# Performance work log

Hardware: AMD Instinct MI355X
Metric: run time of the kernel (lower is better)

The kernel has to match this reference:

```python
import jax, jax.numpy as jnp
import numpy as np

NUM_USER = 262144
NUM_ITEM = 262144
DIM = 64
NNZ = 1_250_000
N_LAYERS = 3


def setup_inputs() -> dict:
    key = jax.random.key(0)
    ku, ki, kr, kc, kv = jax.random.split(key, 5)
    n = NUM_USER + NUM_ITEM
    # xavier_uniform bound for (rows, cols) weight
    a = float(np.sqrt(6.0 / (NUM_USER + DIM)))
    user_emb = jax.random.uniform(ku, (NUM_USER, DIM), minval=-a, maxval=a, dtype=jnp.float32)
    b = float(np.sqrt(6.0 / (NUM_ITEM + DIM)))
    item_emb = jax.random.uniform(ki, (NUM_ITEM, DIM), minval=-b, maxval=b, dtype=jnp.float32)
    adj_rows = jax.random.randint(kr, (NNZ,), 0, n, dtype=jnp.int32)
    adj_cols = jax.random.randint(kc, (NNZ,), 0, n, dtype=jnp.int32)
    # normalized adjacency values are small positive floats
    adj_vals = jax.random.uniform(kv, (NNZ,), minval=0.0, maxval=0.1, dtype=jnp.float32)
    return {"user_emb": user_emb, "item_emb": item_emb,
            "adj_rows": adj_rows, "adj_cols": adj_cols, "adj_vals": adj_vals}


def reference(user_emb, item_emb, adj_rows, adj_cols, adj_vals):
    num_user = user_emb.shape[0]
    ego = jnp.concatenate([user_emb, item_emb], axis=0)  # [N, D]
    n = ego.shape[0]

    def spmm(x):
        # sparse.mm(adj, x): gather source rows, scale, scatter-add to dest rows
        msgs = adj_vals[:, None] * x[adj_cols]            # [NNZ, D]
        return jax.ops.segment_sum(msgs, adj_rows, num_segments=n)

    # running sum instead of stack+mean (same math: mean over L+1 layer outputs)
    acc = ego
    cur = ego
    for _ in range(N_LAYERS):
        cur = spmm(cur)
        acc = acc + cur
    mean_emb = acc / jnp.asarray(N_LAYERS + 1, dtype=ego.dtype)
    return mean_emb[:num_user], mean_emb[num_user:]
```

## Files before the change

### kernel.cpp

```cpp
#include <hip/hip_runtime.h>


constexpr int NUM_USER = 262144;
constexpr int NUM_ITEM = 262144;
constexpr int DIM      = 64;
constexpr int N_NODES  = NUM_USER + NUM_ITEM;
constexpr int NNZ      = 1250000;

constexpr int NBUCK = 256;
constexpr int ROWS_PER_BUCK = N_NODES / NBUCK;
constexpr int PB_BLOCKS = 512;
constexpr int CHUNK = 2444;
constexpr int BCAP = 6144;

typedef float  __f4 __attribute__((ext_vector_type(4)));

__device__ __forceinline__ unsigned bfpack2(float a, float b) {
    unsigned ua = __float_as_uint(a); ua += 0x7fffu + ((ua >> 16) & 1u);
    unsigned ub = __float_as_uint(b); ub += 0x7fffu + ((ub >> 16) & 1u);
    return (ua >> 16) | (ub & 0xffff0000u);
}
__device__ __forceinline__ uint4 bfpack8(float4 a, float4 b) {
    return make_uint4(bfpack2(a.x, a.y), bfpack2(a.z, a.w),
                      bfpack2(b.x, b.y), bfpack2(b.z, b.w));
}
__device__ __forceinline__ void bfunpack8(uint4 u, float4& l, float4& h) {
    l.x = __uint_as_float(u.x << 16);
    l.y = __uint_as_float(u.x & 0xffff0000u);
    l.z = __uint_as_float(u.y << 16);
    l.w = __uint_as_float(u.y & 0xffff0000u);
    h.x = __uint_as_float(u.z << 16);
    h.y = __uint_as_float(u.z & 0xffff0000u);
    h.z = __uint_as_float(u.w << 16);
    h.w = __uint_as_float(u.w & 0xffff0000u);
}
__device__ __forceinline__ void fma4(float4& s, float v, const float4 x) {
    s.x = fmaf(v, x.x, s.x);
    s.y = fmaf(v, x.y, s.y);
    s.z = fmaf(v, x.z, s.z);
    s.w = fmaf(v, x.w, s.w);
}
__device__ __forceinline__ float4 add4(float4 a, float4 b) {
    return make_float4(a.x + b.x, a.y + b.y, a.z + b.z, a.w + b.w);
}

__global__ void bucket_count(const int* __restrict__ rows, int* __restrict__ bcnt) {
    __shared__ int lcnt[NBUCK];
    const int t = threadIdx.x;
    lcnt[t] = 0;
    __syncthreads();
    const int beg = blockIdx.x * CHUNK;
    const int end = min(beg + CHUNK, NNZ);
    const int n    = max(end - beg, 0);
    const int nvec = n >> 2;
    const int4* rows4 = (const int4*)(rows + beg);
    for (int i = t; i < nvec; i += 256) {
        const int4 r = rows4[i];
        atomicAdd(&lcnt[r.x >> 11], 1);
        atomicAdd(&lcnt[r.y >> 11], 1);
        atomicAdd(&lcnt[r.z >> 11], 1);
        atomicAdd(&lcnt[r.w >> 11], 1);
    }
    if (t < (n & 3)) atomicAdd(&lcnt[rows[beg + (nvec << 2) + t] >> 11], 1);
    __syncthreads();
    bcnt[t * PB_BLOCKS + blockIdx.x] = lcnt[t];
}

__global__ void scan_bcnt(int* __restrict__ bcnt, int* __restrict__ tot) {
    __shared__ int tmp[256];
    const int b = blockIdx.x, t = threadIdx.x;
    const int a0 = bcnt[b * PB_BLOCKS + 2 * t];
    const int a1 = bcnt[b * PB_BLOCKS + 2 * t + 1];
    const int run = a0 + a1;
    tmp[t] = run;
    __syncthreads();
    for (int off = 1; off < 256; off <<= 1) {
        int x = (t >= off) ? tmp[t - off] : 0;
        __syncthreads();
        tmp[t] += x;
        __syncthreads();
    }
    const int excl = tmp[t] - run;
    bcnt[b * PB_BLOCKS + 2 * t]     = excl;
    bcnt[b * PB_BLOCKS + 2 * t + 1] = excl + a0;
    if (t == 255) tot[b] = tmp[255];
}

__global__ void scan_btot(const int* __restrict__ tot, int* __restrict__ bbase) {
    __shared__ int tmp[256];
    const int t = threadIdx.x;
    const int v = tot[t];
    tmp[t] = v;
    __syncthreads();
    for (int off = 1; off < 256; off <<= 1) {
        int x = (t >= off) ? tmp[t - off] : 0;
        __syncthreads();
        tmp[t] += x;
        __syncthreads();
    }
    bbase[t] = tmp[t] - v;
    if (t == 0) bbase[NBUCK] = NNZ;
}

__global__ void bucket_scatter(const int* __restrict__ rows, const int* __restrict__ cols,
                               const float* __restrict__ vals,
                               const int* __restrict__ bcnt, const int* __restrict__ bbase,
                               int2* __restrict__ eb, unsigned short* __restrict__ ebrow) {
    __shared__ int lbase[NBUCK];
    __shared__ int lofs[NBUCK];
    const int t = threadIdx.x;
    lbase[t] = bbase[t] + bcnt[t * PB_BLOCKS + blockIdx.x];
    lofs[t] = 0;
    __syncthreads();
    const int beg = blockIdx.x * CHUNK;
    const int end = min(beg + CHUNK, NNZ);
    const int n    = max(end - beg, 0);
    const int nvec = n >> 2;
    const int4*   rows4 = (const int4*)(rows + beg);
    const int4*   cols4 = (const int4*)(cols + beg);
    const float4* vals4 = (const float4*)(vals + beg);
    for (int i = t; i < nvec; i += 256) {
        const int4   r = rows4[i];
        const int4   c = cols4[i];
        const float4 v = vals4[i];
        int b, p;
        b = r.x >> 11; p = lbase[b] + atomicAdd(&lofs[b], 1);
        eb[p] = make_int2(c.x, __float_as_int(v.x));
        ebrow[p] = (unsigned short)(r.x & (ROWS_PER_BUCK - 1));
        b = r.y >> 11; p = lbase[b] + atomicAdd(&lofs[b], 1);
        eb[p] = make_int2(c.y, __float_as_int(v.y));
        ebrow[p] = (unsigned short)(r.y & (ROWS_PER_BUCK - 1));
        b = r.z >> 11; p = lbase[b] + atomicAdd(&lofs[b], 1);
        eb[p] = make_int2(c.z, __float_as_int(v.z));
        ebrow[p] = (unsigned short)(r.z & (ROWS_PER_BUCK - 1));
        b = r.w >> 11; p = lbase[b] + atomicAdd(&lofs[b], 1);
        eb[p] = make_int2(c.w, __float_as_int(v.w));
        ebrow[p] = (unsigned short)(r.w & (ROWS_PER_BUCK - 1));
    }
    if (t < (n & 3)) {
        const int i = beg + (nvec << 2) + t;
        const int r = rows[i];
        const int b = r >> 11;
        const int p = lbase[b] + atomicAdd(&lofs[b], 1);
        eb[p] = make_int2(cols[i], __float_as_int(vals[i]));
        ebrow[p] = (unsigned short)(r & (ROWS_PER_BUCK - 1));
    }
}

__global__ void bucket_finalize(const int* __restrict__ bbase,
                                const int2* __restrict__ eb,
                                const unsigned short* __restrict__ ebrow,
                                int* __restrict__ row_ptr, int2* __restrict__ sc) {
    __shared__ int  lcnt[ROWS_PER_BUCK];
    __shared__ int  tmp[256];
    __shared__ int2 lout[BCAP];
    const int b    = blockIdx.x;
    const int t    = threadIdx.x;
    const int base = bbase[b];
    const int cnt  = bbase[b + 1] - base;
    for (int r = t; r < ROWS_PER_BUCK; r += 256) lcnt[r] = 0;
    __syncthreads();
    for (int i = t; i < cnt; i += 256)
        atomicAdd(&lcnt[ebrow[base + i]], 1);
    __syncthreads();
    int loc[8];
    int run = 0;
    #pragma unroll
    for (int k = 0; k < 8; ++k) { const int v = lcnt[t * 8 + k]; loc[k] = run; run += v; }
    tmp[t] = run;
    __syncthreads();
    for (int off = 1; off < 256; off <<= 1) {
        int x = (t >= off) ? tmp[t - off] : 0;
        __syncthreads();
        tmp[t] += x;
        __syncthreads();
    }
    const int excl = tmp[t] - run;
    #pragma unroll
    for (int k = 0; k < 8; ++k) lcnt[t * 8 + k] = loc[k] + excl;
    __syncthreads();
    for (int r = t; r < ROWS_PER_BUCK; r += 256)
        row_ptr[b * ROWS_PER_BUCK + r] = base + lcnt[r];
    if (b == NBUCK - 1 && t == 0) row_ptr[N_NODES] = NNZ;
    __syncthreads();
    if (cnt <= BCAP) {
        for (int i = t; i < cnt; i += 256) {
            const int p = atomicAdd(&lcnt[ebrow[base + i]], 1);
            lout[p] = eb[base + i];
        }
        __syncthreads();
        for (int i = t; i < cnt; i += 256)
            sc[base + i] = lout[i];
    } else {
        for (int i = t; i < cnt; i += 256) {
            const int p = atomicAdd(&lcnt[ebrow[base + i]], 1);
            sc[base + p] = eb[base + i];
        }
    }
}

__global__ void spmm_first(const int* __restrict__ ptr, const int2* __restrict__ sc,
                           const float4* __restrict__ ue4, const float4* __restrict__ ie4,
                           uint4* __restrict__ e1b) {
    const int row = blockIdx.x * 32 + (threadIdx.x >> 3);
    const int d8  = threadIdx.x & 7;
    const int beg = ptr[row];
    const int end = ptr[row + 1];
    float4 a0 = {0.f,0.f,0.f,0.f}, b0 = {0.f,0.f,0.f,0.f};
    float4 a1 = {0.f,0.f,0.f,0.f}, b1 = {0.f,0.f,0.f,0.f};
    int e = beg;
    for (; e + 2 <= end; e += 2) {
        const int2 A = sc[e];
        const int2 B = sc[e + 1];
        const float4* pa = (A.x < NUM_USER) ? ue4 + (size_t)A.x * 16
                                            : ie4 + (size_t)(A.x - NUM_USER) * 16;
        const float4* pb = (B.x < NUM_USER) ? ue4 + (size_t)B.x * 16
                                            : ie4 + (size_t)(B.x - NUM_USER) * 16;
        const float4 al = pa[2 * d8], ah = pa[2 * d8 + 1];
        const float4 bl = pb[2 * d8], bh = pb[2 * d8 + 1];
        const float va = __int_as_float(A.y);
        const float vb = __int_as_float(B.y);
        fma4(a0, va, al); fma4(b0, va, ah);
        fma4(a1, vb, bl); fma4(b1, vb, bh);
    }
    if (e < end) {
        const int2 A = sc[e];
        const float4* pa = (A.x < NUM_USER) ? ue4 + (size_t)A.x * 16
                                            : ie4 + (size_t)(A.x - NUM_USER) * 16;
        const float va = __int_as_float(A.y);
        fma4(a0, va, pa[2 * d8]); fma4(b0, va, pa[2 * d8 + 1]);
    }
    e1b[row * 8 + d8] = bfpack8(add4(a0, a1), add4(b0, b1));
}

__global__ void spmm_b2b(const int* __restrict__ ptr, const int2* __restrict__ sc,
                         const uint4* __restrict__ xb, uint4* __restrict__ yb) {
    const int row = blockIdx.x * 32 + (threadIdx.x >> 3);
    const int d8  = threadIdx.x & 7;
    const int beg = ptr[row];
    const int end = ptr[row + 1];
    float4 a0 = {0.f,0.f,0.f,0.f}, b0 = {0.f,0.f,0.f,0.f};
    float4 a1 = {0.f,0.f,0.f,0.f}, b1 = {0.f,0.f,0.f,0.f};
    int e = beg;
    for (; e + 2 <= end; e += 2) {
        const int2 A = sc[e];
        const int2 B = sc[e + 1];
        const uint4 xa = xb[A.x * 8 + d8];
        const uint4 xc = xb[B.x * 8 + d8];
        float4 l, h;
        bfunpack8(xa, l, h);
        fma4(a0, __int_as_float(A.y), l); fma4(b0, __int_as_float(A.y), h);
        bfunpack8(xc, l, h);
        fma4(a1, __int_as_float(B.y), l); fma4(b1, __int_as_float(B.y), h);
    }
    if (e < end) {
        const int2 A = sc[e];
        float4 l, h;
        bfunpack8(xb[A.x * 8 + d8], l, h);
        fma4(a0, __int_as_float(A.y), l); fma4(b0, __int_as_float(A.y), h);
    }
    yb[row * 8 + d8] = bfpack8(add4(a0, a1), add4(b0, b1));
}

__global__ void spmm_last(const int* __restrict__ ptr, const int2* __restrict__ sc,
                          const float4* __restrict__ ue4, const float4* __restrict__ ie4,
                          const uint4* __restrict__ e1b, const uint4* __restrict__ e2b,
                          float4* __restrict__ out4) {
    const int row = blockIdx.x * 32 + (threadIdx.x >> 3);
    const int d8  = threadIdx.x & 7;
    const int beg = ptr[row];
    const int end = ptr[row + 1];
    const int o8 = row * 8 + d8;
    const float4* pg = (row < NUM_USER) ? ue4 + (size_t)row * 16
                                        : ie4 + (size_t)(row - NUM_USER) * 16;
    const float4 gl = pg[2 * d8];
    const float4 gh = pg[2 * d8 + 1];
    const uint4 u1 = e1b[o8];
    const uint4 u2 = e2b[o8];
    float4 a0 = {0.f,0.f,0.f,0.f}, b0 = {0.f,0.f,0.f,0.f};
    float4 a1 = {0.f,0.f,0.f,0.f}, b1 = {0.f,0.f,0.f,0.f};
    int e = beg;
    for (; e + 2 <= end; e += 2) {
        const int2 A = sc[e];
        const int2 B = sc[e + 1];
        const uint4 xa = e2b[A.x * 8 + d8];
        const uint4 xc = e2b[B.x * 8 + d8];
        float4 l, h;
        bfunpack8(xa, l, h);
        fma4(a0, __int_as_float(A.y), l); fma4(b0, __int_as_float(A.y), h);
        bfunpack8(xc, l, h);
        fma4(a1, __int_as_float(B.y), l); fma4(b1, __int_as_float(B.y), h);
    }
    if (e < end) {
        const int2 A = sc[e];
        float4 l, h;
        bfunpack8(e2b[A.x * 8 + d8], l, h);
        fma4(a0, __int_as_float(A.y), l); fma4(b0, __int_as_float(A.y), h);
    }
    a0 = add4(a0, a1); b0 = add4(b0, b1);
    float4 l1, h1, l2, h2;
    bfunpack8(u1, l1, h1);
    bfunpack8(u2, l2, h2);
    float4 r0, r1;
    r0.x = (gl.x + l1.x + l2.x + a0.x) * 0.25f;
    r0.y = (gl.y + l1.y + l2.y + a0.y) * 0.25f;
    r0.z = (gl.z + l1.z + l2.z + a0.z) * 0.25f;
    r0.w = (gl.w + l1.w + l2.w + a0.w) * 0.25f;
    r1.x = (gh.x + h1.x + h2.x + b0.x) * 0.25f;
    r1.y = (gh.y + h1.y + h2.y + b0.y) * 0.25f;
    r1.z = (gh.z + h1.z + h2.z + b0.z) * 0.25f;
    r1.w = (gh.w + h1.w + h2.w + b0.w) * 0.25f;
    __builtin_nontemporal_store(*(const __f4*)&r0, (__f4*)&out4[row * 16 + 2 * d8]);
    __builtin_nontemporal_store(*(const __f4*)&r1, (__f4*)&out4[row * 16 + 2 * d8 + 1]);
}

__global__ void lgcn_init(const float4* __restrict__ ue, const float4* __restrict__ ie,
                          float4* __restrict__ cur, float4* __restrict__ acc) {
    const long total  = (long)N_NODES * (DIM / 4);
    const long utotal = (long)NUM_USER * (DIM / 4);
    long i = (long)blockIdx.x * blockDim.x + threadIdx.x;
    const long stride = (long)gridDim.x * blockDim.x;
    for (; i < total; i += stride) {
        float4 v = (i < utotal) ? ue[i] : ie[i - utotal];
        cur[i] = v;
        acc[i] = v;
    }
}

__global__ void lgcn_spmm_atomic(const int* __restrict__ rows, const int* __restrict__ cols,
                                 const float* __restrict__ vals, const float* __restrict__ x,
                                 float* __restrict__ y) {
    const long total  = (long)NNZ * DIM;
    long t = (long)blockIdx.x * blockDim.x + threadIdx.x;
    const long stride = (long)gridDim.x * blockDim.x;
    for (; t < total; t += stride) {
        const int e = (int)(t >> 6);
        const int d = (int)(t & 63);
        atomicAdd(&y[((long)rows[e] << 6) + d], vals[e] * x[((long)cols[e] << 6) + d]);
    }
}

__global__ void lgcn_add(float4* __restrict__ acc, const float4* __restrict__ nxt, float scale) {
    const long total  = (long)N_NODES * (DIM / 4);
    long i = (long)blockIdx.x * blockDim.x + threadIdx.x;
    const long stride = (long)gridDim.x * blockDim.x;
    for (; i < total; i += stride) {
        float4 a = acc[i];
        const float4 b = nxt[i];
        a.x = (a.x + b.x) * scale;
        a.y = (a.y + b.y) * scale;
        a.z = (a.z + b.z) * scale;
        a.w = (a.w + b.w) * scale;
        acc[i] = a;
    }
}

extern "C" void kernel_launch(void* const* d_in, const int* in_sizes, int n_in,
                              void* d_out, int out_size, void* d_ws, size_t ws_size,
                              hipStream_t stream) {
    const float* ue   = (const float*)d_in[0];
    const float* ie   = (const float*)d_in[1];
    const int*   rows = (const int*)d_in[2];
    const int*   cols = (const int*)d_in[3];
    const float* vals = (const float*)d_in[4];
    float* out = (float*)d_out;

    const size_t embBytes  = (size_t)N_NODES * DIM * sizeof(float);
    const size_t embBytesH = embBytes / 2;
    char* ws = (char*)d_ws;
    uint4* e1b = (uint4*)ws;
    uint4* e2b = (uint4*)(ws + embBytesH);
    char* p = ws + 2 * embBytesH;
    int2* sc = (int2*)p;                 p += (size_t)NNZ * 8;
    int2* eb = (int2*)p;                 p += (size_t)NNZ * 8;
    unsigned short* ebrow = (unsigned short*)p; p += (size_t)NNZ * 2;
    int* row_ptr = (int*)p;              p += (size_t)(N_NODES + 1) * 4;
    int* bcnt    = (int*)p;              p += (size_t)NBUCK * PB_BLOCKS * 4;
    int* tot     = (int*)p;              p += (size_t)NBUCK * 4;
    int* bbase   = (int*)p;              p += (size_t)(NBUCK + 1) * 4;
    const size_t need = (size_t)(p - ws);

    if (ws_size >= need) {
        bucket_count   <<<PB_BLOCKS, 256, 0, stream>>>(rows, bcnt);
        scan_bcnt      <<<NBUCK,     256, 0, stream>>>(bcnt, tot);
        scan_btot      <<<1,         256, 0, stream>>>(tot, bbase);
        bucket_scatter <<<PB_BLOCKS, 256, 0, stream>>>(rows, cols, vals, bcnt, bbase,
                                                       eb, ebrow);
        bucket_finalize<<<NBUCK,     256, 0, stream>>>(bbase, eb, ebrow, row_ptr, sc);

        spmm_first<<<N_NODES / 32, 256, 0, stream>>>(row_ptr, sc,
                                                     (const float4*)ue, (const float4*)ie,
                                                     e1b);
        spmm_b2b  <<<N_NODES / 32, 256, 0, stream>>>(row_ptr, sc, e1b, e2b);
        spmm_last <<<N_NODES / 32, 256, 0, stream>>>(row_ptr, sc,
                                                     (const float4*)ue, (const float4*)ie,
                                                     e1b, e2b, (float4*)out);
    } else {
        float* buf0 = (float*)ws;
        float* buf1 = (float*)(ws + embBytes);
        lgcn_init<<<4096, 256, 0, stream>>>((const float4*)ue, (const float4*)ie,
                                            (float4*)buf0, (float4*)out);
        float* cur = buf0;
        float* nxt = buf1;
        for (int l = 0; l < 3; ++l) {
            hipMemsetAsync(nxt, 0, embBytes, stream);
            lgcn_spmm_atomic<<<2048, 256, 0, stream>>>(rows, cols, vals, cur, nxt);
            const float scale = (l == 2) ? 0.25f : 1.0f;
            lgcn_add<<<4096, 256, 0, stream>>>((float4*)out, (const float4*)nxt, scale);
            float* t = cur; cur = nxt; nxt = t;
        }
    }
}
```

Before: 241.2 us.

## Sort rows by degree within each bucket to balance SpMM wavefront work

```diff
diff --git a/kernel.cpp b/kernel.cpp
--- a/kernel.cpp
+++ b/kernel.cpp
@@ -12,6 +12,7 @@
 constexpr int PB_BLOCKS = 512;
 constexpr int CHUNK = 2444;
 constexpr int BCAP = 6144;
+constexpr int DEGB = 33;
 
 typedef float  __f4 __attribute__((ext_vector_type(4)));
 
@@ -150,15 +151,20 @@
 __global__ void bucket_finalize(const int* __restrict__ bbase,
                                 const int2* __restrict__ eb,
                                 const unsigned short* __restrict__ ebrow,
-                                int* __restrict__ row_ptr, int2* __restrict__ sc) {
+                                int* __restrict__ row_ptr, int2* __restrict__ sc,
+                                int* __restrict__ perm) {
     __shared__ int  lcnt[ROWS_PER_BUCK];
     __shared__ int  tmp[256];
     __shared__ int2 lout[BCAP];
+    __shared__ unsigned short ldeg[ROWS_PER_BUCK];
+    __shared__ int  dh[DEGB];
+    __shared__ int  dbase[DEGB];
     const int b    = blockIdx.x;
     const int t    = threadIdx.x;
     const int base = bbase[b];
     const int cnt  = bbase[b + 1] - base;
     for (int r = t; r < ROWS_PER_BUCK; r += 256) lcnt[r] = 0;
+    if (t < DEGB) dh[t] = 0;
     __syncthreads();
     for (int i = t; i < cnt; i += 256)
         atomicAdd(&lcnt[ebrow[base + i]], 1);
@@ -179,10 +185,26 @@
     #pragma unroll
     for (int k = 0; k < 8; ++k) lcnt[t * 8 + k] = loc[k] + excl;
     __syncthreads();
-    for (int r = t; r < ROWS_PER_BUCK; r += 256)
-        row_ptr[b * ROWS_PER_BUCK + r] = base + lcnt[r];
+    for (int r = t; r < ROWS_PER_BUCK; r += 256) {
+        const int s = lcnt[r];
+        const int d = ((r == ROWS_PER_BUCK - 1) ? cnt : lcnt[r + 1]) - s;
+        row_ptr[b * ROWS_PER_BUCK + r] = base + s;
+        ldeg[r] = (unsigned short)min(d, DEGB - 1);
+        atomicAdd(&dh[min(d, DEGB - 1)], 1);
+    }
     if (b == NBUCK - 1 && t == 0) row_ptr[N_NODES] = NNZ;
     __syncthreads();
+    if (t == 0) {
+        int s = 0;
+        for (int i = 0; i < DEGB; ++i) { dbase[i] = s; s += dh[i]; }
+    }
+    __syncthreads();
+    if (t < DEGB) dh[t] = dbase[t];
+    __syncthreads();
+    for (int r = t; r < ROWS_PER_BUCK; r += 256) {
+        const int pos = atomicAdd(&dh[ldeg[r]], 1);
+        perm[b * ROWS_PER_BUCK + pos] = b * ROWS_PER_BUCK + r;
+    }
     if (cnt <= BCAP) {
         for (int i = t; i < cnt; i += 256) {
             const int p = atomicAdd(&lcnt[ebrow[base + i]], 1);
@@ -200,9 +222,10 @@
 }
 
 __global__ void spmm_first(const int* __restrict__ ptr, const int2* __restrict__ sc,
+                           const int* __restrict__ perm,
                            const float4* __restrict__ ue4, const float4* __restrict__ ie4,
                            uint4* __restrict__ e1b) {
-    const int row = blockIdx.x * 32 + (threadIdx.x >> 3);
+    const int row = perm[blockIdx.x * 32 + (threadIdx.x >> 3)];
     const int d8  = threadIdx.x & 7;
     const int beg = ptr[row];
     const int end = ptr[row + 1];
@@ -234,8 +257,9 @@
 }
 
 __global__ void spmm_b2b(const int* __restrict__ ptr, const int2* __restrict__ sc,
+                         const int* __restrict__ perm,
                          const uint4* __restrict__ xb, uint4* __restrict__ yb) {
-    const int row = blockIdx.x * 32 + (threadIdx.x >> 3);
+    const int row = perm[blockIdx.x * 32 + (threadIdx.x >> 3)];
     const int d8  = threadIdx.x & 7;
     const int beg = ptr[row];
     const int end = ptr[row + 1];
@@ -263,10 +287,11 @@
 }
 
 __global__ void spmm_last(const int* __restrict__ ptr, const int2* __restrict__ sc,
+                          const int* __restrict__ perm,
                           const float4* __restrict__ ue4, const float4* __restrict__ ie4,
                           const uint4* __restrict__ e1b, const uint4* __restrict__ e2b,
                           float4* __restrict__ out4) {
-    const int row = blockIdx.x * 32 + (threadIdx.x >> 3);
+    const int row = perm[blockIdx.x * 32 + (threadIdx.x >> 3)];
     const int d8  = threadIdx.x & 7;
     const int beg = ptr[row];
     const int end = ptr[row + 1];
@@ -375,6 +400,7 @@
     int2* eb = (int2*)p;                 p += (size_t)NNZ * 8;
     unsigned short* ebrow = (unsigned short*)p; p += (size_t)NNZ * 2;
     int* row_ptr = (int*)p;              p += (size_t)(N_NODES + 1) * 4;
+    int* perm    = (int*)p;              p += (size_t)N_NODES * 4;
     int* bcnt    = (int*)p;              p += (size_t)NBUCK * PB_BLOCKS * 4;
     int* tot     = (int*)p;              p += (size_t)NBUCK * 4;
     int* bbase   = (int*)p;              p += (size_t)(NBUCK + 1) * 4;
@@ -386,13 +412,14 @@
         scan_btot      <<<1,         256, 0, stream>>>(tot, bbase);
         bucket_scatter <<<PB_BLOCKS, 256, 0, stream>>>(rows, cols, vals, bcnt, bbase,
                                                        eb, ebrow);
-        bucket_finalize<<<NBUCK,     256, 0, stream>>>(bbase, eb, ebrow, row_ptr, sc);
-
-        spmm_first<<<N_NODES / 32, 256, 0, stream>>>(row_ptr, sc,
+        bucket_finalize<<<NBUCK,     256, 0, stream>>>(bbase, eb, ebrow, row_ptr, sc,
+                                                       perm);
+
+        spmm_first<<<N_NODES / 32, 256, 0, stream>>>(row_ptr, sc, perm,
                                                      (const float4*)ue, (const float4*)ie,
                                                      e1b);
-        spmm_b2b  <<<N_NODES / 32, 256, 0, stream>>>(row_ptr, sc, e1b, e2b);
-        spmm_last <<<N_NODES / 32, 256, 0, stream>>>(row_ptr, sc,
+        spmm_b2b  <<<N_NODES / 32, 256, 0, stream>>>(row_ptr, sc, perm, e1b, e2b);
+        spmm_last <<<N_NODES / 32, 256, 0, stream>>>(row_ptr, sc, perm,
                                                      (const float4*)ue, (const float4*)ie,
                                                      e1b, e2b, (float4*)out);
     } else {
```

After: 269.1 us. 11.6% more time.
